# Kernel optimization log

Measured on AMD Instinct MI355X. Metric: run time of the kernel, lower is better.

## Reference

```python
import jax, jax.numpy as jnp
import numpy as np
from math import factorial

N_NODES = 10000
N_EDGES = 320000
FEAT = 32
NBASIS = 8
RMAX = 6.0
ZMAX = 119


def _cg(j1, m1, j2, m2, j3, m3):
    if m1 + m2 != m3 or j3 < abs(j1 - j2) or j3 > j1 + j2:
        return 0.0
    f = lambda n: float(factorial(n))
    pre = ((2 * j3 + 1) * f(j1 + j2 - j3) * f(j1 - j2 + j3) * f(-j1 + j2 + j3) / f(j1 + j2 + j3 + 1)) ** 0.5
    pre *= (f(j3 + m3) * f(j3 - m3) * f(j1 - m1) * f(j1 + m1) * f(j2 - m2) * f(j2 + m2)) ** 0.5
    s = 0.0
    for k in range(j1 + j2 + j3 + 1):
        d = [k, j1 + j2 - j3 - k, j1 - m1 - k, j2 + m2 - k, j3 - j2 + m1 + k, j3 - j1 - m2 + k]
        if min(d) < 0:
            continue
        s += (-1) ** k / (f(d[0]) * f(d[1]) * f(d[2]) * f(d[3]) * f(d[4]) * f(d[5]))
    return pre * s


def _u_real(l):
    # complex->real spherical harmonics unitary transform
    U = np.zeros((2 * l + 1, 2 * l + 1), dtype=complex)
    s2 = 1.0 / np.sqrt(2.0)
    for m in range(-l, l + 1):
        i = m + l
        if m == 0:
            U[i, l] = 1.0
        elif m > 0:
            U[i, l + m] = ((-1) ** m) * s2
            U[i, l - m] = s2
        else:
            U[i, l + m] = 1j * s2
            U[i, l - m] = -1j * ((-1) ** m) * s2
    return U


def _real_cg():
    # real Clebsch-Gordan coupling coefficients for l<=2, shape (9,9,9), sparse
    off = [0, 1, 4]
    C = np.zeros((9, 9, 9))
    Us = [_u_real(l) for l in range(3)]
    for l1 in range(3):
        for l2 in range(3):
            for l3 in range(3):
                if l3 < abs(l1 - l2) or l3 > l1 + l2:
                    continue
                cg = np.zeros((2 * l1 + 1, 2 * l2 + 1, 2 * l3 + 1))
                for m1 in range(-l1, l1 + 1):
                    for m2 in range(-l2, l2 + 1):
                        m3 = m1 + m2
                        if abs(m3) <= l3:
                            cg[m1 + l1, m2 + l2, m3 + l3] = _cg(l1, m1, l2, m2, l3, m3)
                blk = np.einsum('ia,jb,kc,abc->ijk', Us[l1], Us[l2], np.conj(Us[l3]), cg.astype(complex))
                C[off[l1]:off[l1] + 2 * l1 + 1, off[l2]:off[l2] + 2 * l2 + 1, off[l3]:off[l3] + 2 * l3 + 1] = blk.real + blk.imag
    return C

CGC = jnp.asarray(_real_cg(), dtype=jnp.float32)
SL = [slice(0, 1), slice(1, 4), slice(4, 9)]
PATHS0 = [(0, 0, 0), (0, 1, 1), (0, 2, 2)]
PATHS1 = [(l1, l2, l3) for l1 in range(3) for l2 in range(3) for l3 in range(3) if abs(l1 - l2) <= l3 <= l1 + l2]
PATHS2 = [(0, 0, 0), (1, 1, 0), (2, 2, 0)]


def _real_sph(u):
    x, y, z = u[:, 0], u[:, 1], u[:, 2]
    c0 = 0.28209479177387814
    c1 = 0.4886025119029199
    c2a = 1.0925484305920792
    c2b = 0.31539156525252005
    c2c = 0.5462742152960396
    return jnp.stack([c0 * jnp.ones_like(x), c1 * y, c1 * z, c1 * x,
                      c2a * x * y, c2a * y * z, c2b * (3.0 * z * z - 1.0), c2a * x * z,
                      c2c * (x * x - y * y)], axis=-1)


def _message_pass(x, rad, Y, src, dst, W, paths, out_dim, n_nodes):
    # gather src node features -> per-edge CG tensor product with (radial x Ylm) basis -> scatter-add to dst
    xs = x[src, 0]  # (E, Dx, F)
    msg = jnp.zeros((rad.shape[0], out_dim, x.shape[-1]), x.dtype)
    for p, (l1, l2, l3) in enumerate(paths):
        w = rad @ W[p]  # (E, F) learned radial path weights
        contrib = jnp.einsum('abc,eaf,eb,ef->ecf', CGC[SL[l1], SL[l2], SL[l3]], xs[:, SL[l1], :], Y[:, SL[l2]], w)
        msg = msg.at[:, SL[l3], :].add(contrib)
    y = jax.ops.segment_sum(msg, dst, num_segments=n_nodes)
    return y[:, None]  # (N, 1, out_dim, F)


def _eadd(a, b):
    if a.shape[2] == b.shape[2]:
        return a + b
    if a.shape[2] < b.shape[2]:
        a, b = b, a
    return a.at[:, :, :b.shape[2], :].add(b)


def _edense(x, K, b):
    # equivariant Dense: shared kernel across degrees, bias only on scalar (l=0) channel
    y = jnp.einsum('npdf,fg->npdg', x, K)
    return y.at[:, :, 0, :].add(b)


def _esilu(x):
    # silu on scalars, sigmoid(scalar)-gated scaling on l>0 components (equivariant)
    if x.shape[2] == 1:
        return jax.nn.silu(x)
    s = x[:, :, 0:1, :]
    return jnp.concatenate([jax.nn.silu(s), x[:, :, 1:, :] * jax.nn.sigmoid(s)], axis=2)


def _forward(dr_vec, Z, neighbor_idxs, embed, wmp0, wmp1, wmp2, dk1, db1, dk2, db2):
    idx_i, idx_j = neighbor_idxs[0], neighbor_idxs[1]
    nN = Z.shape[0]
    r = jnp.sqrt(jnp.sum(dr_vec * dr_vec, axis=-1) + 1e-12)  # (E,)
    u = dr_vec / r[:, None]
    n = jnp.arange(1, NBASIS + 1, dtype=dr_vec.dtype)
    rad = jnp.sqrt(2.0 / RMAX) * jnp.sin(n * jnp.pi * r[:, None] / RMAX) / r[:, None]  # Bessel radial basis
    t = jnp.clip(r / RMAX, 0.0, 1.0 - 1e-6)
    cut = jnp.where(r < RMAX, jnp.exp(1.0 - 1.0 / (1.0 - t * t)), 0.0)  # smooth cutoff
    mask = (idx_i != idx_j).astype(dr_vec.dtype)  # mask padding/self edges
    rad = rad * (cut * mask)[:, None]
    Y = _real_sph(u)  # (E, 9)
    x = embed[Z][:, None, None, :]  # (N, 1, 1, F)
    for it, (paths, W) in enumerate([(PATHS0, wmp0), (PATHS1, wmp1), (PATHS2, wmp2)]):
        last = it == 2
        y = _message_pass(x, rad, Y, idx_j, idx_i, W, paths, 1 if last else 9, nN)
        if last:
            x = x[:, :, 0:1, :]  # change_max_degree_or_type -> scalars only
        y = _eadd(x, y)
        y = _edense(y, dk1[it], db1[it])
        y = _esilu(y)
        y = _edense(y, dk2[it], db2[it])
        x = _eadd(x, y)
    return x[:, 0, 0, :]


def setup_inputs():
    key = jax.random.key(0)
    ks = jax.random.split(key, 10)
    dr_vec = 2.0 * jax.random.normal(ks[0], (N_EDGES, 3), jnp.float32)
    Z = jax.random.randint(ks[1], (N_NODES,), 0, ZMAX)
    neighbor_idxs = jax.random.randint(ks[2], (2, N_EDGES), 0, N_NODES)
    embed = jax.random.normal(ks[3], (ZMAX, FEAT), jnp.float32)
    sB = 1.0 / np.sqrt(NBASIS)
    wmp0 = sB * jax.random.normal(ks[4], (len(PATHS0), NBASIS, FEAT), jnp.float32)
    wmp1 = sB * jax.random.normal(ks[5], (len(PATHS1), NBASIS, FEAT), jnp.float32)
    wmp2 = sB * jax.random.normal(ks[6], (len(PATHS2), NBASIS, FEAT), jnp.float32)
    sF = 1.0 / np.sqrt(FEAT)
    dense_k1 = sF * jax.random.normal(ks[7], (3, FEAT, FEAT), jnp.float32)
    dense_b1 = jnp.zeros((3, FEAT), jnp.float32)
    dense_k2 = 0.1 * sF * jax.random.normal(ks[8], (3, FEAT, FEAT), jnp.float32)
    dense_b2 = jnp.zeros((3, FEAT), jnp.float32)
    return {"dr_vec": dr_vec, "Z": Z, "neighbor_idxs": neighbor_idxs, "embed": embed,
            "wmp0": wmp0, "wmp1": wmp1, "wmp2": wmp2,
            "dense_k1": dense_k1, "dense_b1": dense_b1, "dense_k2": dense_k2, "dense_b2": dense_b2}


def reference(dr_vec, Z, neighbor_idxs, embed, wmp0, wmp1, wmp2, dense_k1, dense_b1, dense_k2, dense_b2):
    return _forward(dr_vec, Z, neighbor_idxs, embed, wmp0, wmp1, wmp2, dense_k1, dense_b1, dense_k2, dense_b2)
```

## Files before the change

kernel.cpp:

```cpp
#include <hip/hip_runtime.h>
#include <type_traits>
#include <cstdint>
#include <cstddef>

#define N_FEAT 32
#define NBASIS 8
#define SPAN   16
#define BSLOTS 8
#define BEDGES (SPAN*BSLOTS)

namespace cgc {

constexpr double dfact(int n){ double r=1.0; for(int i=2;i<=n;++i) r*=(double)i; return r; }

constexpr double dsqrt(double x){
  if(x<=0.0) return 0.0;
  double g = x>1.0 ? x : 1.0;
  for(int i=0;i<200;++i){ double ng = 0.5*(g + x/g); if(ng==g) break; g=ng; }
  return g;
}

constexpr double cg1(int j1,int m1,int j2,int m2,int j3,int m3){
  int adiff = j1-j2; if(adiff<0) adiff=-adiff;
  if(m1+m2!=m3 || j3<adiff || j3>j1+j2) return 0.0;
  double pre = dsqrt((double)(2*j3+1)*dfact(j1+j2-j3)*dfact(j1-j2+j3)*dfact(-j1+j2+j3)/dfact(j1+j2+j3+1));
  pre = pre*dsqrt(dfact(j3+m3)*dfact(j3-m3)*dfact(j1-m1)*dfact(j1+m1)*dfact(j2-m2)*dfact(j2+m2));
  double s=0.0;
  for(int k=0;k<=j1+j2+j3;++k){
    int d1=j1+j2-j3-k, d2=j1-m1-k, d3=j2+m2-k, d4=j3-j2+m1+k, d5=j3-j1-m2+k;
    if(d1<0||d2<0||d3<0||d4<0||d5<0) continue;
    double term = 1.0/(dfact(k)*dfact(d1)*dfact(d2)*dfact(d3)*dfact(d4)*dfact(d5));
    s += (k&1)? -term : term;
  }
  return pre*s;
}

struct Tab { float v[9][9][9]; };

constexpr Tab make(){
  Tab T{};
  int off[3]={0,1,4};
  double Ure[3][5][5]={}, Uim[3][5][5]={};
  const double s2 = dsqrt(0.5);
  for(int l=0;l<3;++l){
    for(int m=-l;m<=l;++m){
      int i=m+l;
      if(m==0){ Ure[l][i][l]=1.0; }
      else if(m>0){
        Ure[l][i][l+m] = ((m&1)? -1.0:1.0)*s2;
        Ure[l][i][l-m] = s2;
      } else {
        int am=-m;
        Uim[l][i][l+m] = s2;
        Uim[l][i][l-m] = -(((am&1)?-1.0:1.0))*s2;
      }
    }
  }
  for(int l1=0;l1<3;++l1) for(int l2=0;l2<3;++l2) for(int l3=0;l3<3;++l3){
    int lo = l1-l2; if(lo<0) lo=-lo;
    if(l3<lo || l3>l1+l2) continue;
    int d1=2*l1+1, d2=2*l2+1, d3=2*l3+1;
    double cg[5][5][5]={};
    for(int m1=-l1;m1<=l1;++m1) for(int m2=-l2;m2<=l2;++m2){
      int m3=m1+m2;
      if(m3>=-l3 && m3<=l3) cg[m1+l1][m2+l2][m3+l3] = cg1(l1,m1,l2,m2,l3,m3);
    }
    double t1re[5][5][5]={}, t1im[5][5][5]={};
    for(int a=0;a<d1;++a) for(int b=0;b<d2;++b) for(int k=0;k<d3;++k){
      double sre=0, sim=0;
      for(int c=0;c<d3;++c){
        double g=cg[a][b][c]; if(g==0.0) continue;
        sre += g*Ure[l3][k][c];
        sim -= g*Uim[l3][k][c];
      }
      t1re[a][b][k]=sre; t1im[a][b][k]=sim;
    }
    double t2re[5][5][5]={}, t2im[5][5][5]={};
    for(int a=0;a<d1;++a) for(int j=0;j<d2;++j) for(int k=0;k<d3;++k){
      double sre=0,sim=0;
      for(int b=0;b<d2;++b){
        double ur=Ure[l2][j][b], ui=Uim[l2][j][b];
        if(ur==0.0&&ui==0.0) continue;
        sre += ur*t1re[a][b][k]-ui*t1im[a][b][k];
        sim += ur*t1im[a][b][k]+ui*t1re[a][b][k];
      }
      t2re[a][j][k]=sre; t2im[a][j][k]=sim;
    }
    for(int i=0;i<d1;++i) for(int j=0;j<d2;++j) for(int k=0;k<d3;++k){
      double sre=0,sim=0;
      for(int a=0;a<d1;++a){
        double ur=Ure[l1][i][a], ui=Uim[l1][i][a];
        if(ur==0.0&&ui==0.0) continue;
        sre += ur*t2re[a][j][k]-ui*t2im[a][j][k];
        sim += ur*t2im[a][j][k]+ui*t2re[a][j][k];
      }
      T.v[off[l1]+i][off[l2]+j][off[l3]+k] = (float)(sre+sim);
    }
  }
  return T;
}

constexpr Tab T = make();

}

template<int I, int N, typename F>
__device__ __forceinline__ void sfor(F&& f){
  if constexpr (I < N){
    f(std::integral_constant<int,I>{});
    sfor<I+1,N>(static_cast<F&&>(f));
  }
}

constexpr int LOFF[3] = {0,1,4};
constexpr float Y0C = 0.28209479177387814f;

struct PS0 {
  static constexpr int NP=3;
  static constexpr int L[3][3]={{0,0,0},{0,1,1},{0,2,2}};
  static constexpr int ALO=0, AHI=1, OD=9, WOFF=0;
  static constexpr int MINW=4, DEPTH=8;
};
struct PS1a {
  static constexpr int NP=9;
  static constexpr int L[9][3]={{0,0,0},{0,1,1},{0,2,2},
                                {1,0,1},{1,1,0},{1,1,1},{1,1,2},{1,2,1},{1,2,2}};
  static constexpr int ALO=0, AHI=4, OD=9, WOFF=0;
  static constexpr int MINW=3, DEPTH=3;
};
struct PS1b {
  static constexpr int NP=6;
  static constexpr int L[6][3]={{2,0,2},{2,1,1},{2,1,2},{2,2,0},{2,2,1},{2,2,2}};
  static constexpr int ALO=4, AHI=9, OD=9, WOFF=9*NBASIS*N_FEAT;
  static constexpr int MINW=3, DEPTH=3;
};
struct PS2 {
  static constexpr int NP=3;
  static constexpr int L[3][3]={{0,0,0},{1,1,0},{2,2,0}};
  static constexpr int ALO=0, AHI=9, OD=1, WOFF=0;
  static constexpr int MINW=3, DEPTH=3;
};

__global__ void init_kernel(const float* __restrict__ embed, const int* __restrict__ Z,
                            float* __restrict__ xA, int* __restrict__ cnt, int nN){
  int i = blockIdx.x*256 + threadIdx.x;
  if(i >= nN*N_FEAT) return;
  int n = i>>5, f = i&31;
  if(f==0) cnt[n]=0;
  xA[(size_t)n*288 + f] = embed[Z[n]*N_FEAT + f];
}

__global__ void count_kernel(const int* __restrict__ dst, int* __restrict__ cnt, int E){
  int e = blockIdx.x*256 + threadIdx.x;
  if(e<E) atomicAdd(&cnt[dst[e]], 1);
}

__global__ void __launch_bounds__(1024) scan_kernel(const int* __restrict__ cnt,
                                                    int* __restrict__ cursor, int n){
  __shared__ int part[1024];
  const int tid = threadIdx.x;
  const int chunk = (n + 1023) >> 10;
  const int s0 = tid*chunk;
  const int s1 = (s0+chunk < n) ? s0+chunk : n;
  int s=0;
  for(int i=s0;i<s1;++i) s += cnt[i];
  part[tid]=s; __syncthreads();
  for(int off=1; off<1024; off<<=1){
    int v = 0;
    if(tid>=off) v = part[tid-off];
    __syncthreads();
    part[tid] += v;
    __syncthreads();
  }
  int run = part[tid] - s;
  for(int i=s0;i<s1;++i){
    int cv = cnt[i];
    cursor[i]=run;
    run += cv;
  }
}

__global__ void fillgeom_kernel(const int* __restrict__ dst, const int* __restrict__ src,
                                const float* __restrict__ dr, int* __restrict__ cursor,
                                int* __restrict__ srcsP, float* __restrict__ radY, int E){
  int e = blockIdx.x*256 + threadIdx.x;
  if(e>=E) return;
  const int d = dst[e], s = src[e];
  const int pos = atomicAdd(&cursor[d], 1);
  srcsP[pos] = s | (d<<16);

  float dx=dr[3*e], dy=dr[3*e+1], dz=dr[3*e+2];
  float r2 = fmaf(dx,dx,fmaf(dy,dy,fmaf(dz,dz,1e-12f)));
  float r = sqrtf(r2);
  float inv = 1.f/r;
  float ux=dx*inv, uy=dy*inv, uz=dz*inv;
  float t = r*(1.f/6.f);
  t = fminf(fmaxf(t,0.f), 1.f-1e-6f);
  float cut = 0.f;
  if (r < 6.f) cut = __expf(1.f - 1.f/(1.f - t*t));
  if (d==s) cut = 0.f;
  float base = 0.57735026918962576f * inv * cut;
  float* o = radY + (size_t)pos*16;
  const float pir = 0.52359877559829887f * r;
  float sT, cT;
  __sincosf(pir, &sT, &cT);
  const float twoc = 2.f*cT;
  float sp = 0.f, sc = sT;
  o[0] = base*sc;
  #pragma unroll
  for(int nb=2; nb<=8; ++nb){
    float sn = fmaf(twoc, sc, -sp);
    o[nb-1] = base*sn;
    sp = sc; sc = sn;
  }
  o[8]  = 0.4886025119029199f*uy;
  o[9]  = 0.4886025119029199f*uz;
  o[10] = 0.4886025119029199f*ux;
  o[11] = 1.0925484305920792f*ux*uy;
  o[12] = 1.0925484305920792f*uy*uz;
  o[13] = 0.31539156525252005f*(3.f*uz*uz-1.f);
  o[14] = 1.0925484305920792f*ux*uz;
  o[15] = 0.5462742152960396f*(ux*ux-uy*uy);
}

template<class PS>
__device__ __forceinline__ void mp_body(
    int bid, float* sRad, int* sS,
    const int* __restrict__ srcsP, const float* __restrict__ radY,
    const float* __restrict__ x_in, const float* __restrict__ W,
    float* __restrict__ ymsg, int E)
{
  constexpr int NP = PS::NP;
  constexpr int ALO = PS::ALO, AHI = PS::AHI, DA = AHI-ALO;
  constexpr int OD = PS::OD;
  constexpr int DEPTH = PS::DEPTH, NBUF = DEPTH+1;

  const int tid  = threadIdx.x;
  const int base = bid * BEDGES;
  const int nE   = (base + BEDGES <= E) ? BEDGES : (E - base);

  {
    const float4* g4 = (const float4*)(radY + (size_t)base*16);
    float4* s4 = (float4*)sRad;
    const int n4 = nE*4;
    for (int i=tid; i<n4; i+=256) s4[i] = g4[i];
    for (int i=tid; i<nE;  i+=256) sS[i] = srcsP[base+i];
  }
  __syncthreads();

  const int f  = tid & 31;
  const int k0 = (tid>>5)*SPAN;
  if (k0 >= nE) return;

  float Wreg[NP][NBASIS];
  sfor<0,NP>([&](auto P){
    constexpr int p = P.value;
    constexpr bool fold = (PS::L[p][1]==0);
    sfor<0,NBASIS>([&](auto Q){
      float v = W[PS::WOFF + (p*NBASIS+Q.value)*N_FEAT + f];
      if constexpr (fold) v *= Y0C;
      Wreg[p][Q.value] = v;
    });
  });

  float msg[OD];
  sfor<0,OD>([&](auto C){ msg[C.value]=0.f; });

  auto gather = [&](float (&dst)[DA], int k){
    const int s = sS[k] & 0xFFFF;
    const float* xb = x_in + (size_t)s*288 + ALO*N_FEAT + f;
    sfor<0,DA>([&](auto A){ dst[A.value] = xb[A.value*N_FEAT]; });
  };

  auto compute = [&](const float (&xs)[DA], int k){
    const float* rp = sRad + k*16;
    const float4 q0 = *(const float4*)(rp);
    const float4 q1 = *(const float4*)(rp+4);
    const float4 q2 = *(const float4*)(rp+8);
    const float4 q3 = *(const float4*)(rp+12);
    const float rad[8] = {q0.x,q0.y,q0.z,q0.w,q1.x,q1.y,q1.z,q1.w};
    const float Yv[8]  = {q2.x,q2.y,q2.z,q2.w,q3.x,q3.y,q3.z,q3.w};
    sfor<0,NP>([&](auto P){
      constexpr int p  = P.value;
      constexpr int l1 = PS::L[p][0], l2 = PS::L[p][1], l3 = PS::L[p][2];
      constexpr int o1 = LOFF[l1], o2 = LOFF[l2], o3 = LOFF[l3];
      float w = 0.f;
      sfor<0,NBASIS>([&](auto Q){ w = fmaf(rad[Q.value], Wreg[p][Q.value], w); });
      sfor<0,2*l2+1>([&](auto B){
        constexpr int b = B.value;
        float yw;
        if constexpr (l2==0) yw = w;
        else                 yw = Yv[o2+b-1]*w;
        sfor<0,2*l1+1>([&](auto A){
          constexpr int a = A.value;
          sfor<0,2*l3+1>([&](auto C){
            constexpr int c = C.value;
            constexpr float cgv = cgc::T.v[o1+a][o2+b][o3+c];
            if constexpr (cgv > 1e-7f || cgv < -1e-7f){
              msg[o3+c] = fmaf(cgv*xs[o1+a-ALO], yw, msg[o3+c]);
            }
          });
        });
      });
    });
  };

  auto flush = [&](int d){
    float* yb = ymsg + ((size_t)d*OD)*N_FEAT + f;
    sfor<0,OD>([&](auto C){
      atomicAdd(yb + C.value*N_FEAT, msg[C.value]);
      msg[C.value] = 0.f;
    });
  };

  if (nE == BEDGES){
    float buf[NBUF][DA];
    sfor<0,DEPTH>([&](auto J){ gather(buf[J.value], k0 + J.value); });
    int vcur = sS[k0];
    sfor<0,SPAN>([&](auto I){
      constexpr int i = I.value;
      int vnext;
      if constexpr (i+1 < SPAN) vnext = sS[k0+i+1]; else vnext = -1;
      if constexpr (i+DEPTH < SPAN) gather(buf[(i+DEPTH)%NBUF], k0+i+DEPTH);
      compute(buf[i%NBUF], k0+i);
      if (i == SPAN-1 || (vnext>>16) != (vcur>>16)) flush(vcur>>16);
      vcur = vnext;
    });
  } else {
    const int k1 = (k0+SPAN < nE) ? k0+SPAN : nE;
    for (int k=k0; k<k1; ++k){
      float xs[DA];
      gather(xs, k);
      compute(xs, k);
      const int dc = sS[k]>>16;
      const int dn = (k+1 < k1) ? (sS[k+1]>>16) : -1;
      if (dn != dc) flush(dc);
    }
  }
}

template<class PS>
__global__ void __launch_bounds__(256, PS::MINW) mp_kernel(
    const int* __restrict__ srcsP, const float* __restrict__ radY,
    const float* __restrict__ x_in, const float* __restrict__ W,
    float* __restrict__ ymsg, int E)
{
  __shared__ float sRad[BEDGES*16];
  __shared__ int   sS[BEDGES];
  mp_body<PS>(blockIdx.x, sRad, sS, srcsP, radY, x_in, W, ymsg, E);
}

__global__ void __launch_bounds__(256, 3) mp1_kernel(
    const int* __restrict__ srcsP, const float* __restrict__ radY,
    const float* __restrict__ x_in, const float* __restrict__ W,
    float* __restrict__ ymsg, int E, int gMP)
{
  __shared__ float sRad[BEDGES*16];
  __shared__ int   sS[BEDGES];
  const int b = blockIdx.x;
  if (b < gMP) mp_body<PS1a>(b,     sRad, sS, srcsP, radY, x_in, W, ymsg, E);
  else         mp_body<PS1b>(b-gMP, sRad, sS, srcsP, radY, x_in, W, ymsg, E);
}

template<int DX>
__global__ void __launch_bounds__(256) nodeA_kernel(
    const float* __restrict__ xin, const float* __restrict__ ymsg,
    const float* __restrict__ K1, const float* __restrict__ b1,
    const float* __restrict__ K2, const float* __restrict__ b2,
    float* __restrict__ xout, int nN)
{
  __shared__ float sK1[1024], sK2[1024], sb1[32], sb2[32];
  __shared__ float tb[8][9][32];
  const int tid = threadIdx.x;
  for(int i=tid;i<1024;i+=256){ sK1[i]=K1[i]; sK2[i]=K2[i]; }
  if(tid<32){ sb1[tid]=b1[tid]; sb2[tid]=b2[tid]; }
  __syncthreads();
  const int h = tid>>5, f = tid&31;
  const int n = blockIdx.x*8 + h;
  const bool valid = n < nN;
  const int nc = valid ? n : 0;
  float xi[9];
  #pragma unroll
  for(int c=0;c<9;++c){
    float t = ymsg[((size_t)nc*9+c)*32+f];
    float x = 0.f;
    if (c<DX) x = xin[((size_t)nc*9+c)*32+f];
    xi[c]=x;
    tb[h][c][f] = t + x;
  }
  __syncthreads();
  float u[9];
  #pragma unroll
  for(int c=0;c<9;++c){
    float acc = (c==0) ? sb1[f] : 0.f;
    #pragma unroll
    for(int g=0;g<32;++g) acc = fmaf(tb[h][c][g], sK1[g*32+f], acc);
    u[c]=acc;
  }
  const float gate = 1.f/(1.f+expf(-u[0]));
  __syncthreads();
  #pragma unroll
  for(int c=0;c<9;++c) tb[h][c][f] = u[c]*gate;
  __syncthreads();
  #pragma unroll
  for(int c=0;c<9;++c){
    float acc = (c==0) ? sb2[f] : 0.f;
    #pragma unroll
    for(int g=0;g<32;++g) acc = fmaf(tb[h][c][g], sK2[g*32+f], acc);
    if (valid) xout[((size_t)n*9+c)*32+f] = acc + ((c<DX) ? xi[c] : 0.f);
  }
}

__global__ void __launch_bounds__(256) nodeB_kernel(
    const float* __restrict__ xin, const float* __restrict__ msg0,
    const float* __restrict__ K1, const float* __restrict__ b1,
    const float* __restrict__ K2, const float* __restrict__ b2,
    float* __restrict__ out, int nN)
{
  __shared__ float sK1[1024], sK2[1024], sb1[32], sb2[32];
  __shared__ float tb[8][32];
  const int tid = threadIdx.x;
  for(int i=tid;i<1024;i+=256){ sK1[i]=K1[i]; sK2[i]=K2[i]; }
  if(tid<32){ sb1[tid]=b1[tid]; sb2[tid]=b2[tid]; }
  __syncthreads();
  const int h = tid>>5, f = tid&31;
  const int n = blockIdx.x*8 + h;
  const bool valid = n < nN;
  const int nc = valid ? n : 0;
  const float x0 = xin[(size_t)nc*288 + f];
  tb[h][f] = msg0[(size_t)nc*32+f] + x0;
  __syncthreads();
  float acc = sb1[f];
  #pragma unroll
  for(int g=0;g<32;++g) acc = fmaf(tb[h][g], sK1[g*32+f], acc);
  const float gate = 1.f/(1.f+expf(-acc));
  const float v = acc*gate;
  __syncthreads();
  tb[h][f] = v;
  __syncthreads();
  float acc2 = sb2[f];
  #pragma unroll
  for(int g=0;g<32;++g) acc2 = fmaf(tb[h][g], sK2[g*32+f], acc2);
  if (valid) out[(size_t)n*32+f] = x0 + acc2;
}

extern "C" void kernel_launch(void* const* d_in, const int* in_sizes, int n_in,
                              void* d_out, int out_size, void* d_ws, size_t ws_size,
                              hipStream_t stream) {
  const float* dr    = (const float*)d_in[0];
  const int*   Z     = (const int*)  d_in[1];
  const int*   nbr   = (const int*)  d_in[2];
  const float* embed = (const float*)d_in[3];
  const float* wmp0  = (const float*)d_in[4];
  const float* wmp1  = (const float*)d_in[5];
  const float* wmp2  = (const float*)d_in[6];
  const float* dk1   = (const float*)d_in[7];
  const float* db1   = (const float*)d_in[8];
  const float* dk2   = (const float*)d_in[9];
  const float* db2   = (const float*)d_in[10];
  const int nN = in_sizes[1];
  const int E  = in_sizes[2]/2;
  const int* idx_i = nbr;
  const int* idx_j = nbr + E;

  uintptr_t base = (uintptr_t)d_ws;
  auto alloc = [&](size_t bytes)->void*{
    uintptr_t p = (base + 255) & ~(uintptr_t)255;
    base = p + bytes;
    return (void*)p;
  };
  float* radY    = (float*)alloc((size_t)E*16*4);
  int*   cnt     = (int*)  alloc((size_t)nN*4);
  int*   cursor  = (int*)  alloc((size_t)nN*4);
  int*   srcsP   = (int*)  alloc((size_t)E*4);
  float* xA      = (float*)alloc((size_t)nN*288*4);
  float* xB      = (float*)alloc((size_t)nN*288*4);
  float* ymsg    = (float*)alloc((size_t)nN*288*4);

  const int gE  = (E+255)/256;
  const int gI  = (nN*N_FEAT+255)/256;
  const int gND = (nN+7)/8;
  const int gMP = (E + BEDGES - 1) / BEDGES;
  const size_t ymsgBytes = (size_t)nN*288*4;

  init_kernel    <<<gI, 256, 0, stream>>>(embed, Z, xA, cnt, nN);
  count_kernel   <<<gE, 256, 0, stream>>>(idx_i, cnt, E);
  scan_kernel    <<<1, 1024, 0, stream>>>(cnt, cursor, nN);
  fillgeom_kernel<<<gE, 256, 0, stream>>>(idx_i, idx_j, dr, cursor, srcsP, radY, E);

  hipMemsetAsync(ymsg, 0, ymsgBytes, stream);
  mp_kernel<PS0><<<gMP, 256, 0, stream>>>(srcsP, radY, xA, wmp0, ymsg, E);
  nodeA_kernel<1><<<gND, 256, 0, stream>>>(xA, ymsg, dk1, db1, dk2, db2, xB, nN);
  hipMemsetAsync(ymsg, 0, ymsgBytes, stream);
  mp1_kernel<<<2*gMP, 256, 0, stream>>>(srcsP, radY, xB, wmp1, ymsg, E, gMP);
  nodeA_kernel<9><<<gND, 256, 0, stream>>>(xB, ymsg, dk1+1024, db1+32, dk2+1024, db2+32, xA, nN);
  hipMemsetAsync(ymsg, 0, (size_t)nN*32*4, stream);
  mp_kernel<PS2><<<gMP, 256, 0, stream>>>(srcsP, radY, xA, wmp2, ymsg, E);
  nodeB_kernel<<<gND, 256, 0, stream>>>(xA, ymsg, dk1+2048, db1+64, dk2+2048, db2+64,
                                        (float*)d_out, nN);
}
```

Before: 409.0 us.

## Gather layer-0 features from embedding table and merge layer-1 path halves per block

Layer-0 message passing now reads source features from the small embedding table, indexed by a per-edge atomic number byte that fillgeom stores, instead of from the 288-float node rows. The layer-1 kernel no longer launches two block halves that each stage radial and index data into shared memory. Each block now runs both path groups in sequence over the same staged edges, which halves the staging traffic and block count. The trade-off is a longer per-block critical path, higher register pressure from two phases in one kernel, and an extra byte array written during geometry fill. The tail condition also changes from a per-block full-tile test to a per-warp-span test.

Result: slower. 450.2 us (+10.1%).

```diff
diff --git a/kernel.cpp b/kernel.cpp
--- a/kernel.cpp
+++ b/kernel.cpp
@@ -120,6 +120,7 @@
   static constexpr int L[3][3]={{0,0,0},{0,1,1},{0,2,2}};
   static constexpr int ALO=0, AHI=1, OD=9, WOFF=0;
   static constexpr int MINW=4, DEPTH=8;
+  static constexpr bool EMB=true;
 };
 struct PS1a {
   static constexpr int NP=9;
@@ -127,18 +128,21 @@
                                 {1,0,1},{1,1,0},{1,1,1},{1,1,2},{1,2,1},{1,2,2}};
   static constexpr int ALO=0, AHI=4, OD=9, WOFF=0;
   static constexpr int MINW=3, DEPTH=3;
+  static constexpr bool EMB=false;
 };
 struct PS1b {
   static constexpr int NP=6;
   static constexpr int L[6][3]={{2,0,2},{2,1,1},{2,1,2},{2,2,0},{2,2,1},{2,2,2}};
   static constexpr int ALO=4, AHI=9, OD=9, WOFF=9*NBASIS*N_FEAT;
   static constexpr int MINW=3, DEPTH=3;
+  static constexpr bool EMB=false;
 };
 struct PS2 {
   static constexpr int NP=3;
   static constexpr int L[3][3]={{0,0,0},{1,1,0},{2,2,0}};
   static constexpr int ALO=0, AHI=9, OD=1, WOFF=0;
   static constexpr int MINW=3, DEPTH=3;
+  static constexpr bool EMB=false;
 };
 
 __global__ void init_kernel(const float* __restrict__ embed, const int* __restrict__ Z,
@@ -181,13 +185,16 @@
 }
 
 __global__ void fillgeom_kernel(const int* __restrict__ dst, const int* __restrict__ src,
-                                const float* __restrict__ dr, int* __restrict__ cursor,
-                                int* __restrict__ srcsP, float* __restrict__ radY, int E){
+                                const int* __restrict__ Z, const float* __restrict__ dr,
+                                int* __restrict__ cursor, int* __restrict__ srcsP,
+                                unsigned char* __restrict__ zsrc,
+                                float* __restrict__ radY, int E){
   int e = blockIdx.x*256 + threadIdx.x;
   if(e>=E) return;
   const int d = dst[e], s = src[e];
   const int pos = atomicAdd(&cursor[d], 1);
   srcsP[pos] = s | (d<<16);
+  zsrc[pos]  = (unsigned char)Z[s];
 
   float dx=dr[3*e], dy=dr[3*e+1], dz=dr[3*e+2];
   float r2 = fmaf(dx,dx,fmaf(dy,dy,fmaf(dz,dz,1e-12f)));
@@ -224,33 +231,15 @@
 }
 
 template<class PS>
-__device__ __forceinline__ void mp_body(
-    int bid, float* sRad, int* sS,
-    const int* __restrict__ srcsP, const float* __restrict__ radY,
-    const float* __restrict__ x_in, const float* __restrict__ W,
-    float* __restrict__ ymsg, int E)
+__device__ __forceinline__ void mp_phase(
+    int k0, int nE, const float* sRad, const int* sS, const unsigned char* sZb,
+    const float* __restrict__ x_in, const float* __restrict__ emb,
+    const float* __restrict__ W, float* __restrict__ ymsg, int f)
 {
   constexpr int NP = PS::NP;
   constexpr int ALO = PS::ALO, AHI = PS::AHI, DA = AHI-ALO;
   constexpr int OD = PS::OD;
   constexpr int DEPTH = PS::DEPTH, NBUF = DEPTH+1;
-
-  const int tid  = threadIdx.x;
-  const int base = bid * BEDGES;
-  const int nE   = (base + BEDGES <= E) ? BEDGES : (E - base);
-
-  {
-    const float4* g4 = (const float4*)(radY + (size_t)base*16);
-    float4* s4 = (float4*)sRad;
-    const int n4 = nE*4;
-    for (int i=tid; i<n4; i+=256) s4[i] = g4[i];
-    for (int i=tid; i<nE;  i+=256) sS[i] = srcsP[base+i];
-  }
-  __syncthreads();
-
-  const int f  = tid & 31;
-  const int k0 = (tid>>5)*SPAN;
-  if (k0 >= nE) return;
 
   float Wreg[NP][NBASIS];
   sfor<0,NP>([&](auto P){
@@ -267,9 +256,14 @@
   sfor<0,OD>([&](auto C){ msg[C.value]=0.f; });
 
   auto gather = [&](float (&dst)[DA], int k){
-    const int s = sS[k] & 0xFFFF;
-    const float* xb = x_in + (size_t)s*288 + ALO*N_FEAT + f;
-    sfor<0,DA>([&](auto A){ dst[A.value] = xb[A.value*N_FEAT]; });
+    if constexpr (PS::EMB){
+      const int zs = sZb[k];
+      dst[0] = emb[zs*N_FEAT + f];
+    } else {
+      const int s = sS[k] & 0xFFFF;
+      const float* xb = x_in + (size_t)s*288 + ALO*N_FEAT + f;
+      sfor<0,DA>([&](auto A){ dst[A.value] = xb[A.value*N_FEAT]; });
+    }
   };
 
   auto compute = [&](const float (&xs)[DA], int k){
@@ -313,7 +307,7 @@
     });
   };
 
-  if (nE == BEDGES){
+  if (k0 + SPAN <= nE){
     float buf[NBUF][DA];
     sfor<0,DEPTH>([&](auto J){ gather(buf[J.value], k0 + J.value); });
     int vcur = sS[k0];
@@ -339,27 +333,60 @@
   }
 }
 
+template<bool EMB>
+__device__ __forceinline__ int mp_stage(
+    int bid, float* sRad, int* sS, unsigned char* sZb,
+    const int* __restrict__ srcsP, const unsigned char* __restrict__ zsrc,
+    const float* __restrict__ radY, int E)
+{
+  const int tid  = threadIdx.x;
+  const int base = bid * BEDGES;
+  const int nE   = (base + BEDGES <= E) ? BEDGES : (E - base);
+  {
+    const float4* g4 = (const float4*)(radY + (size_t)base*16);
+    float4* s4 = (float4*)sRad;
+    const int n4 = nE*4;
+    for (int i=tid; i<n4; i+=256) s4[i] = g4[i];
+    for (int i=tid; i<nE;  i+=256) sS[i] = srcsP[base+i];
+    if constexpr (EMB){
+      for (int i=tid; i<nE; i+=256) sZb[i] = zsrc[base+i];
+    }
+  }
+  __syncthreads();
+  return nE;
+}
+
 template<class PS>
 __global__ void __launch_bounds__(256, PS::MINW) mp_kernel(
+    const int* __restrict__ srcsP, const unsigned char* __restrict__ zsrc,
+    const float* __restrict__ radY, const float* __restrict__ x_in,
+    const float* __restrict__ emb, const float* __restrict__ W,
+    float* __restrict__ ymsg, int E)
+{
+  __shared__ float sRad[BEDGES*16];
+  __shared__ int   sS[BEDGES];
+  __shared__ unsigned char sZb[BEDGES];
+  const int nE = mp_stage<PS::EMB>(blockIdx.x, sRad, sS, sZb, srcsP, zsrc, radY, E);
+  const int f  = threadIdx.x & 31;
+  const int k0 = (threadIdx.x>>5)*SPAN;
+  if (k0 >= nE) return;
+  mp_phase<PS>(k0, nE, sRad, sS, sZb, x_in, emb, W, ymsg, f);
+}
+
+__global__ void __launch_bounds__(256, 3) mp1_kernel(
     const int* __restrict__ srcsP, const float* __restrict__ radY,
     const float* __restrict__ x_in, const float* __restrict__ W,
     float* __restrict__ ymsg, int E)
 {
   __shared__ float sRad[BEDGES*16];
   __shared__ int   sS[BEDGES];
-  mp_body<PS>(blockIdx.x, sRad, sS, srcsP, radY, x_in, W, ymsg, E);
-}
-
-__global__ void __launch_bounds__(256, 3) mp1_kernel(
-    const int* __restrict__ srcsP, const float* __restrict__ radY,
-    const float* __restrict__ x_in, const float* __restrict__ W,
-    float* __restrict__ ymsg, int E, int gMP)
-{
-  __shared__ float sRad[BEDGES*16];
-  __shared__ int   sS[BEDGES];
-  const int b = blockIdx.x;
-  if (b < gMP) mp_body<PS1a>(b,     sRad, sS, srcsP, radY, x_in, W, ymsg, E);
-  else         mp_body<PS1b>(b-gMP, sRad, sS, srcsP, radY, x_in, W, ymsg, E);
+  const int nE = mp_stage<false>(blockIdx.x, sRad, sS, nullptr, srcsP, nullptr, radY, E);
+  const int f  = threadIdx.x & 31;
+  const int k0 = (threadIdx.x>>5)*SPAN;
+  if (k0 >= nE) return;
+  mp_phase<PS1a>(k0, nE, sRad, sS, nullptr, x_in, nullptr, W, ymsg, f);
+  __builtin_amdgcn_sched_barrier(0);
+  mp_phase<PS1b>(k0, nE, sRad, sS, nullptr, x_in, nullptr, W, ymsg, f);
 }
 
 template<int DX>
@@ -473,6 +500,7 @@
   int*   cnt     = (int*)  alloc((size_t)nN*4);
   int*   cursor  = (int*)  alloc((size_t)nN*4);
   int*   srcsP   = (int*)  alloc((size_t)E*4);
+  unsigned char* zsrc = (unsigned char*)alloc((size_t)E);
   float* xA      = (float*)alloc((size_t)nN*288*4);
   float* xB      = (float*)alloc((size_t)nN*288*4);
   float* ymsg    = (float*)alloc((size_t)nN*288*4);
@@ -486,16 +514,16 @@
   init_kernel    <<<gI, 256, 0, stream>>>(embed, Z, xA, cnt, nN);
   count_kernel   <<<gE, 256, 0, stream>>>(idx_i, cnt, E);
   scan_kernel    <<<1, 1024, 0, stream>>>(cnt, cursor, nN);
-  fillgeom_kernel<<<gE, 256, 0, stream>>>(idx_i, idx_j, dr, cursor, srcsP, radY, E);
+  fillgeom_kernel<<<gE, 256, 0, stream>>>(idx_i, idx_j, Z, dr, cursor, srcsP, zsrc, radY, E);
 
   hipMemsetAsync(ymsg, 0, ymsgBytes, stream);
-  mp_kernel<PS0><<<gMP, 256, 0, stream>>>(srcsP, radY, xA, wmp0, ymsg, E);
+  mp_kernel<PS0><<<gMP, 256, 0, stream>>>(srcsP, zsrc, radY, xA, embed, wmp0, ymsg, E);
   nodeA_kernel<1><<<gND, 256, 0, stream>>>(xA, ymsg, dk1, db1, dk2, db2, xB, nN);
   hipMemsetAsync(ymsg, 0, ymsgBytes, stream);
-  mp1_kernel<<<2*gMP, 256, 0, stream>>>(srcsP, radY, xB, wmp1, ymsg, E, gMP);
+  mp1_kernel<<<gMP, 256, 0, stream>>>(srcsP, radY, xB, wmp1, ymsg, E);
   nodeA_kernel<9><<<gND, 256, 0, stream>>>(xB, ymsg, dk1+1024, db1+32, dk2+1024, db2+32, xA, nN);
   hipMemsetAsync(ymsg, 0, (size_t)nN*32*4, stream);
-  mp_kernel<PS2><<<gMP, 256, 0, stream>>>(srcsP, radY, xA, wmp2, ymsg, E);
+  mp_kernel<PS2><<<gMP, 256, 0, stream>>>(srcsP, zsrc, radY, xA, embed, wmp2, ymsg, E);
   nodeB_kernel<<<gND, 256, 0, stream>>>(xA, ymsg, dk1+2048, db1+64, dk2+2048, db2+64,
                                         (float*)d_out, nN);
 }
```
